# Kernel tuning notes

Measured on AMD Instinct MI355X. Metric: run time of the kernel, lower is better.

## Reference

```python
import jax, jax.numpy as jnp
import numpy as np

# LightweightConv1d config (matches init_kwargs)
C = 1024        # input_size / channels
H = 16          # num_heads
K = 7           # kernel_size (odd)
PAD = 3         # padding (same-length output)


def setup_inputs() -> dict:
    key = jax.random.key(0)
    kx, kw = jax.random.split(key)
    x = jax.random.normal(kx, (8, 4096, C), dtype=jnp.float32)   # B x T x C
    weight = jax.random.uniform(kw, (H, 1, K), dtype=jnp.float32)  # per-head kernel
    return {"x": x, "weight": weight}


def reference(x, weight):
    # x: (B, T, C); weight: (H, 1, K)
    B, T, _ = x.shape
    # weight softmax over the kernel dimension (weight_softmax=True)
    w = jax.nn.softmax(weight.reshape(H, K), axis=-1)  # (H, K)
    # weight_dropout is identity at inference (eval mode)
    # channel c uses head c % H -> tile head kernels C//H times along channel axis
    w_chan = jnp.tile(w, (C // H, 1))[:, None, :]      # (C, 1, K) depthwise kernel
    x_nct = jnp.transpose(x, (0, 2, 1))                # (B, C, T)
    y = jax.lax.conv_general_dilated(
        x_nct, w_chan,
        window_strides=(1,),
        padding=[(PAD, PAD)],
        dimension_numbers=("NCH", "OIH", "NCH"),
        feature_group_count=C,
    )                                                  # (B, C, T), same length
    return jnp.transpose(y, (0, 2, 1))                 # (B, T, C)
```

## Files before the change

### kernel.cpp

```cpp
#include <hip/hip_runtime.h>


constexpr int B_   = 8;
constexpr int T_   = 4096;
constexpr int C_   = 1024;
constexpr int H_   = 16;
constexpr int K_   = 7;
constexpr int PAD_ = 3;
constexpr int TCHUNK = 8;
constexpr int W_  = TCHUNK + K_ - 1;
constexpr int C4  = C_ / 4;
constexpr int NCHUNK = T_ / TCHUNK;
constexpr int NXCD = 8;

typedef float vfloat4 __attribute__((ext_vector_type(4)));

__global__ __launch_bounds__(256, 4) void lwconv_kernel(
    const float* __restrict__ x, const float* __restrict__ w,
    float* __restrict__ y) {
  __shared__ float ws[H_][K_];
  const int tid = threadIdx.x;

  if (tid < H_) {
    float v[K_];
    float m = -1e30f;
#pragma unroll
    for (int k = 0; k < K_; ++k) { v[k] = w[tid * K_ + k]; m = fmaxf(m, v[k]); }
    float s = 0.f;
#pragma unroll
    for (int k = 0; k < K_; ++k) { v[k] = expf(v[k] - m); s += v[k]; }
    const float inv = 1.f / s;
#pragma unroll
    for (int k = 0; k < K_; ++k) ws[tid][k] = v[k] * inv;
  }
  __syncthreads();

  const int cpx = (B_ * NCHUNK) / NXCD;
  const int wid = ((int)blockIdx.x % NXCD) * cpx + (int)blockIdx.x / NXCD;
  const int b  = wid / NCHUNK;
  const int t0 = (wid % NCHUNK) * TCHUNK;

  const int h0 = (4 * tid) & (H_ - 1);
  float wr[4][K_];
#pragma unroll
  for (int j = 0; j < 4; ++j)
#pragma unroll
    for (int k = 0; k < K_; ++k) wr[j][k] = ws[h0 + j][k];

  const float4* __restrict__ xr =
      reinterpret_cast<const float4*>(x + (size_t)b * T_ * C_) + tid;
  vfloat4* __restrict__ yr =
      reinterpret_cast<vfloat4*>(y + (size_t)b * T_ * C_) + tid;

  const float4 z4 = make_float4(0.f, 0.f, 0.f, 0.f);

  float4 win[W_];
#pragma unroll
  for (int i = 0; i < W_; ++i) {
    const int t = t0 - PAD_ + i;
    win[i] = (t >= 0 && t < T_) ? xr[(size_t)t * C4] : z4;
  }
#pragma unroll
  for (int i = 0; i < W_; ++i)
    asm volatile("" :: "v"(win[i].x), "v"(win[i].y), "v"(win[i].z), "v"(win[i].w));

#pragma unroll
  for (int tt = 0; tt < TCHUNK; ++tt) {
    float ax = 0.f, ay = 0.f, az = 0.f, aw = 0.f;
#pragma unroll
    for (int k = 0; k < K_; ++k) {
      ax = fmaf(win[tt + k].x, wr[0][k], ax);
      ay = fmaf(win[tt + k].y, wr[1][k], ay);
      az = fmaf(win[tt + k].z, wr[2][k], az);
      aw = fmaf(win[tt + k].w, wr[3][k], aw);
    }
    vfloat4 out;
    out.x = ax; out.y = ay; out.z = az; out.w = aw;
    __builtin_nontemporal_store(out, yr + (size_t)(t0 + tt) * C4);
  }
}

extern "C" void kernel_launch(void* const* d_in, const int* in_sizes, int n_in,
                              void* d_out, int out_size, void* d_ws, size_t ws_size,
                              hipStream_t stream) {
  const float* x = (const float*)d_in[0];
  const float* w = (const float*)d_in[1];
  float* y = (float*)d_out;

  const int grid = B_ * NCHUNK;
  lwconv_kernel<<<grid, 256, 0, stream>>>(x, w, y);
}
```

Measured before the change: 253.5 us.

## Stage input window via direct global-to-LDS loads and per-thread softmax

Replaces the register-resident input window with a shared-memory tile filled by global_load_lds (direct global-to-LDS DMA), zero-filling padding rows at sequence edges. Each thread now computes the softmax weights for its own four heads in registers, which removes the shared weight table and its barrier. The intent is to cut vector register pressure and let loads issue asynchronously, at the cost of a 57 KB LDS tile, fewer blocks per CU (launch bounds lowered from 4 to 2), an LDS read pass and a full wait plus barrier before compute.

```diff
diff --git a/kernel.cpp b/kernel.cpp
--- a/kernel.cpp
+++ b/kernel.cpp
@@ -1,4 +1,5 @@
 #include <hip/hip_runtime.h>
+#include <stdint.h>
 
 
 constexpr int B_   = 8;
@@ -9,74 +10,86 @@
 constexpr int PAD_ = 3;
 constexpr int TCHUNK = 8;
 constexpr int W_  = TCHUNK + K_ - 1;
-constexpr int C4  = C_ / 4;
 constexpr int NCHUNK = T_ / TCHUNK;
 constexpr int NXCD = 8;
 
 typedef float vfloat4 __attribute__((ext_vector_type(4)));
+typedef const __attribute__((address_space(1))) unsigned int* gptr_u32;
+typedef __attribute__((address_space(3))) unsigned int* lptr_u32;
 
-__global__ __launch_bounds__(256, 4) void lwconv_kernel(
+__global__ __launch_bounds__(256, 2) void lwconv_kernel(
     const float* __restrict__ x, const float* __restrict__ w,
     float* __restrict__ y) {
-  __shared__ float ws[H_][K_];
+  __shared__ float xs[W_][C_];
   const int tid = threadIdx.x;
 
-  if (tid < H_) {
+  const int h0 = (4 * tid) & (H_ - 1);
+  float wr[4][K_];
+#pragma unroll
+  for (int j = 0; j < 4; ++j) {
+    const int h = h0 + j;
     float v[K_];
     float m = -1e30f;
 #pragma unroll
-    for (int k = 0; k < K_; ++k) { v[k] = w[tid * K_ + k]; m = fmaxf(m, v[k]); }
+    for (int k = 0; k < K_; ++k) { v[k] = w[h * K_ + k]; m = fmaxf(m, v[k]); }
     float s = 0.f;
 #pragma unroll
     for (int k = 0; k < K_; ++k) { v[k] = expf(v[k] - m); s += v[k]; }
     const float inv = 1.f / s;
 #pragma unroll
-    for (int k = 0; k < K_; ++k) ws[tid][k] = v[k] * inv;
+    for (int k = 0; k < K_; ++k) wr[j][k] = v[k] * inv;
   }
-  __syncthreads();
 
   const int cpx = (B_ * NCHUNK) / NXCD;
   const int wid = ((int)blockIdx.x % NXCD) * cpx + (int)blockIdx.x / NXCD;
   const int b  = wid / NCHUNK;
   const int t0 = (wid % NCHUNK) * TCHUNK;
 
-  const int h0 = (4 * tid) & (H_ - 1);
-  float wr[4][K_];
+  const size_t base = (size_t)b * T_ * C_;
+  const float* xg = x + base + 4 * tid;
+  float*       yg = y + base + 4 * tid;
+
+  const vfloat4 z4 = {0.f, 0.f, 0.f, 0.f};
+  if (t0 == 0) {
 #pragma unroll
-  for (int j = 0; j < 4; ++j)
+    for (int i = 0; i < PAD_; ++i)
+      *reinterpret_cast<vfloat4*>(&xs[i][4 * tid]) = z4;
+  }
+  if (t0 == T_ - TCHUNK) {
 #pragma unroll
-    for (int k = 0; k < K_; ++k) wr[j][k] = ws[h0 + j][k];
+    for (int i = W_ - PAD_; i < W_; ++i)
+      *reinterpret_cast<vfloat4*>(&xs[i][4 * tid]) = z4;
+  }
 
-  const float4* __restrict__ xr =
-      reinterpret_cast<const float4*>(x + (size_t)b * T_ * C_) + tid;
-  vfloat4* __restrict__ yr =
-      reinterpret_cast<vfloat4*>(y + (size_t)b * T_ * C_) + tid;
-
-  const float4 z4 = make_float4(0.f, 0.f, 0.f, 0.f);
-
-  float4 win[W_];
+  const int wq = tid >> 6;
 #pragma unroll
   for (int i = 0; i < W_; ++i) {
     const int t = t0 - PAD_ + i;
-    win[i] = (t >= 0 && t < T_) ? xr[(size_t)t * C4] : z4;
+    if (t >= 0 && t < T_) {
+      __builtin_amdgcn_global_load_lds(
+          (gptr_u32)(xg + (size_t)t * C_),
+          (lptr_u32)&xs[i][wq * 256], 16, 0, 0);
+    }
   }
-#pragma unroll
-  for (int i = 0; i < W_; ++i)
-    asm volatile("" :: "v"(win[i].x), "v"(win[i].y), "v"(win[i].z), "v"(win[i].w));
+
+  asm volatile("s_waitcnt vmcnt(0)" ::: "memory");
+  __syncthreads();
 
 #pragma unroll
   for (int tt = 0; tt < TCHUNK; ++tt) {
     float ax = 0.f, ay = 0.f, az = 0.f, aw = 0.f;
 #pragma unroll
     for (int k = 0; k < K_; ++k) {
-      ax = fmaf(win[tt + k].x, wr[0][k], ax);
-      ay = fmaf(win[tt + k].y, wr[1][k], ay);
-      az = fmaf(win[tt + k].z, wr[2][k], az);
-      aw = fmaf(win[tt + k].w, wr[3][k], aw);
+      const float4 v = *reinterpret_cast<const float4*>(&xs[tt + k][4 * tid]);
+      ax = fmaf(v.x, wr[0][k], ax);
+      ay = fmaf(v.y, wr[1][k], ay);
+      az = fmaf(v.z, wr[2][k], az);
+      aw = fmaf(v.w, wr[3][k], aw);
     }
-    vfloat4 out;
-    out.x = ax; out.y = ay; out.z = az; out.w = aw;
-    __builtin_nontemporal_store(out, yr + (size_t)(t0 + tt) * C4);
+    vfloat4 o;
+    o.x = ax; o.y = ay; o.z = az; o.w = aw;
+    __builtin_nontemporal_store(
+        o, reinterpret_cast<vfloat4*>(yg + (size_t)(t0 + tt) * C_));
   }
 }
 
```

New measurement: 230.8 us. 1.1x faster.
